# Optimization experiments

Measured on AMD Instinct MI355X. Metric: run time of the kernel, lower is better.

## Reference

```python
import jax, jax.numpy as jnp
import numpy as np

TOTAL_TOKENS = 2_000_000
N_READS = 2000
DIM_HIDDEN = 128
VOCAB = 4


def setup_inputs() -> dict:
    key = jax.random.key(0)
    k1, k2, k3 = jax.random.split(key, 3)
    tokens = jax.random.randint(k1, (TOTAL_TOKENS,), 0, VOCAB, dtype=jnp.int64 if jax.config.jax_enable_x64 else jnp.int32)
    segment_ids = jnp.sort(jax.random.randint(k2, (TOTAL_TOKENS,), 0, N_READS, dtype=jnp.int32))
    embedding = jax.random.normal(k3, (VOCAB, DIM_HIDDEN), dtype=jnp.float32)
    return {"tokens": tokens, "segment_ids": segment_ids, "embedding": embedding, "n_reads": N_READS}


def reference(tokens, segment_ids, embedding, n_reads):
    # Per-read: gather base embeddings then mean over the read -> segment-mean.
    gathered = embedding[tokens]                                   # [T, D]
    sums = jax.ops.segment_sum(gathered, segment_ids, num_segments=n_reads)   # [R, D]
    counts = jax.ops.segment_sum(jnp.ones_like(tokens, dtype=embedding.dtype),
                                 segment_ids, num_segments=n_reads)           # [R]
    counts = jnp.maximum(counts, 1.0)  # guard empty segments (torch loop never has empty reads)
    return sums / counts[:, None]
```

## Files before the change

### kernel.cpp

```cpp
#include <hip/hip_runtime.h>
#include <stdint.h>


#define DIM 128
#define TPB 256

__device__ __forceinline__ int wave_lower_bound(const int* __restrict__ a,
                                                int n, int t) {
  const int lane = threadIdx.x & 63;
  int lo = 0, hi = n;
  while (hi - lo > 64) {
    const long long span = hi - lo;
    const int idx = lo + (int)((span * (lane + 1)) >> 6);
    const int probe = (idx < hi) ? a[idx] : 0x7fffffff;
    const unsigned long long mask = __ballot(probe >= t);
    const int first = __ffsll(mask) - 1;
    const int nlo = (first == 0) ? lo : lo + (int)((span * (long long)first) >> 6);
    const int nhi = lo + (int)((span * (long long)(first + 1)) >> 6);
    lo = nlo;
    hi = nhi;
  }
  const int idx = lo + lane;
  const bool ge = (idx < hi) ? (a[idx] >= t) : true;
  const unsigned long long mask = __ballot(ge);
  return lo + __ffsll(mask) - 1;
}

__global__ __launch_bounds__(TPB) void seg_mean_kernel(
    const int* __restrict__ tokens, const int* __restrict__ segs,
    const float* __restrict__ emb, float* __restrict__ out, int T) {
  const int s = blockIdx.x;
  const int tid = threadIdx.x;
  const int wave = tid >> 6;

  __shared__ int bounds[2];
  __shared__ unsigned long long red[TPB / 64];

  if (wave < 2) {
    const int r = wave_lower_bound(segs, T, s + wave);
    if ((tid & 63) == 0) bounds[wave] = r;
  }
  __syncthreads();
  const int lo = bounds[0];
  const int hi = bounds[1];

  unsigned long long acc = 0ULL;
  for (int i = lo + tid; i < hi; i += TPB) {
    acc += 1ULL << ((tokens[i] & 3) << 4);
  }

#pragma unroll
  for (int off = 32; off > 0; off >>= 1) {
    acc += __shfl_down(acc, off, 64);
  }
  if ((tid & 63) == 0) red[wave] = acc;
  __syncthreads();
  if (tid == 0) {
    red[0] = red[0] + red[1] + red[2] + red[3];
  }
  __syncthreads();

  const unsigned long long c = red[0];
  if (tid < DIM) {
    const float c0 = (float)(unsigned)(c & 0xFFFFULL);
    const float c1 = (float)(unsigned)((c >> 16) & 0xFFFFULL);
    const float c2 = (float)(unsigned)((c >> 32) & 0xFFFFULL);
    const float c3 = (float)(unsigned)((c >> 48) & 0xFFFFULL);
    const float tot = fmaxf(c0 + c1 + c2 + c3, 1.0f);
    const float v = c0 * emb[tid] + c1 * emb[DIM + tid] +
                    c2 * emb[2 * DIM + tid] + c3 * emb[3 * DIM + tid];
    out[(long long)s * DIM + tid] = v / tot;
  }
}

extern "C" void kernel_launch(void* const* d_in, const int* in_sizes, int n_in,
                              void* d_out, int out_size, void* d_ws,
                              size_t ws_size, hipStream_t stream) {
  const int* tokens = (const int*)d_in[0];
  const int* segs = (const int*)d_in[1];
  const float* emb = (const float*)d_in[2];
  float* out = (float*)d_out;

  const int T = in_sizes[0];
  const int n_reads = out_size / DIM;

  seg_mean_kernel<<<n_reads, TPB, 0, stream>>>(tokens, segs, emb, out, T);
}
```

Baseline: 71.36 us.

## Bracket segment-boundary search with interpolated guess and remap blocks across XCDs

The lower-bound search now starts from an interpolated guess (t*T/n_reads) and a ±4096 bracket that is checked with two loads, falling back to a full search if the bracket misses. This cuts the number of dependent ballot/probe rounds on the segment array. The final stage scans 256 elements with four loads per lane and a shuffle-min reduction, and block indices are permuted so that consecutive segments land on the same XCD. The gain depends on segment ids being roughly uniform, and the fallback keeps the result correct.

```diff
diff --git a/kernel.cpp b/kernel.cpp
--- a/kernel.cpp
+++ b/kernel.cpp
@@ -1,18 +1,19 @@
 #include <hip/hip_runtime.h>
 #include <stdint.h>
+#include <limits.h>
 
 
 #define DIM 128
 #define TPB 256
+#define BRACKET 4096
 
-__device__ __forceinline__ int wave_lower_bound(const int* __restrict__ a,
-                                                int n, int t) {
+__device__ __forceinline__ int wave_lb(const int* __restrict__ a, int lo,
+                                       int hi, int t) {
   const int lane = threadIdx.x & 63;
-  int lo = 0, hi = n;
-  while (hi - lo > 64) {
+  while (hi - lo > 256) {
     const long long span = hi - lo;
     const int idx = lo + (int)((span * (lane + 1)) >> 6);
-    const int probe = (idx < hi) ? a[idx] : 0x7fffffff;
+    const int probe = (idx < hi) ? a[idx] : INT_MAX;
     const unsigned long long mask = __ballot(probe >= t);
     const int first = __ffsll(mask) - 1;
     const int nlo = (first == 0) ? lo : lo + (int)((span * (long long)first) >> 6);
@@ -20,16 +21,29 @@
     lo = nlo;
     hi = nhi;
   }
-  const int idx = lo + lane;
-  const bool ge = (idx < hi) ? (a[idx] >= t) : true;
-  const unsigned long long mask = __ballot(ge);
-  return lo + __ffsll(mask) - 1;
+  int pos = hi;
+#pragma unroll
+  for (int j = 0; j < 4; ++j) {
+    const int idx = lo + lane * 4 + j;
+    if (idx < hi && a[idx] >= t && idx < pos) pos = idx;
+  }
+#pragma unroll
+  for (int off = 1; off < 64; off <<= 1) {
+    pos = min(pos, __shfl_xor(pos, off, 64));
+  }
+  return pos;
 }
 
 __global__ __launch_bounds__(TPB) void seg_mean_kernel(
     const int* __restrict__ tokens, const int* __restrict__ segs,
-    const float* __restrict__ emb, float* __restrict__ out, int T) {
-  const int s = blockIdx.x;
+    const float* __restrict__ emb, float* __restrict__ out, int T,
+    int n_reads) {
+  int s = blockIdx.x;
+  if ((gridDim.x & 7) == 0) {
+    const int per = gridDim.x >> 3;
+    s = (int)(blockIdx.x & 7) * per + (int)(blockIdx.x >> 3);
+  }
+
   const int tid = threadIdx.x;
   const int wave = tid >> 6;
 
@@ -37,7 +51,19 @@
   __shared__ unsigned long long red[TPB / 64];
 
   if (wave < 2) {
-    const int r = wave_lower_bound(segs, T, s + wave);
+    const int t = s + wave;
+    const int g = (int)(((long long)t * T) / n_reads);
+    int blo = g - BRACKET;
+    if (blo < 0) blo = 0;
+    int bhi = g + BRACKET;
+    if (bhi > T) bhi = T;
+    const bool okl = (blo == 0) || (segs[blo] < t);
+    const bool okr = (bhi == T) || (segs[bhi] >= t);
+    if (!(okl && okr)) {
+      blo = 0;
+      bhi = T;
+    }
+    const int r = wave_lb(segs, blo, bhi, t);
     if ((tid & 63) == 0) bounds[wave] = r;
   }
   __syncthreads();
@@ -84,5 +110,6 @@
   const int T = in_sizes[0];
   const int n_reads = out_size / DIM;
 
-  seg_mean_kernel<<<n_reads, TPB, 0, stream>>>(tokens, segs, emb, out, T);
+  seg_mean_kernel<<<n_reads, TPB, 0, stream>>>(tokens, segs, emb, out, T,
+                                               n_reads);
 }
```

Result: slower. 75.02 us (+5.1%).
